# Kernel optimization log

Hardware: AMD Instinct MI355X
Metric: run time of the kernel (lower is better)

The kernel has to match this reference:

```python
import math
import jax, jax.numpy as jnp
import numpy as np

EMBED_DIM = 1024
D_K = 1024
D_V = 1024


def setup_inputs() -> dict:
    key = jax.random.key(0)
    ks = jax.random.split(key, 7)
    s = 1.0 / math.sqrt(EMBED_DIM)
    return {
        "x": jax.random.normal(ks[0], (4, 2048, EMBED_DIM), dtype=jnp.float32),
        "Wq": jax.random.normal(ks[1], (EMBED_DIM, D_K), dtype=jnp.float32) * s,
        "bq": jax.random.normal(ks[2], (D_K,), dtype=jnp.float32) * 0.01,
        "Wk": jax.random.normal(ks[3], (EMBED_DIM, D_K), dtype=jnp.float32) * s,
        "bk": jax.random.normal(ks[4], (D_K,), dtype=jnp.float32) * 0.01,
        "Wv": jax.random.normal(ks[5], (EMBED_DIM, D_V), dtype=jnp.float32) * s,
        "bv": jax.random.normal(ks[6], (D_V,), dtype=jnp.float32) * 0.01,
    }


def reference(x, Wq, bq, Wk, bk, Wv, bv):
    # x: [B, S, E]
    q = x @ Wq + bq  # [B, S, Dk]
    k = x @ Wk + bk  # [B, S, Dk]
    v = x @ Wv + bv  # [B, S, Dv]
    scores = jnp.einsum('bqd,bkd->bqk', q, k) / jnp.sqrt(jnp.float32(q.shape[-1]))
    # NOTE: softmax over axis=1 (the QUERY axis), matching torch dim=1 on [B,S,S]
    attn = jax.nn.softmax(scores, axis=1)
    return jnp.einsum('bqk,bkv->bqv', attn, v)  # [B, S, Dv]
```

## Files before the change

### kernel.cpp

```cpp
#include <hip/hip_runtime.h>
#include <math.h>

typedef unsigned short ushort_t;
typedef __attribute__((ext_vector_type(8))) short short8;
typedef __attribute__((ext_vector_type(8))) _Float16 half8;
typedef __attribute__((ext_vector_type(4))) float floatx4;

#define BATCH 4
#define SEQ   2048
#define EMB   1024

#define GBM 128
#define GBN 128
#define GBK 32

__device__ __forceinline__ ushort_t f2bf(float f) {
    unsigned u = __float_as_uint(f);
    u += 0x7fff + ((u >> 16) & 1);
    return (ushort_t)(u >> 16);
}
__device__ __forceinline__ float bf2f(ushort_t h) {
    return __uint_as_float(((unsigned)h) << 16);
}
__device__ __forceinline__ ushort_t f2h_bits(float f) {
    _Float16 h = (_Float16)f;
    return __builtin_bit_cast(ushort_t, h);
}
__device__ __forceinline__ float h2f(ushort_t b) {
    return (float)__builtin_bit_cast(_Float16, b);
}

__device__ __forceinline__ void gl_lds16(const ushort_t* g, ushort_t* l) {
    __builtin_amdgcn_global_load_lds(
        (const __attribute__((address_space(1))) void*)g,
        (__attribute__((address_space(3))) void*)l,
        16, 0, 0);
}

__device__ __forceinline__ float wave_reduce_sum(float v) {
    #pragma unroll
    for (int off = 32; off; off >>= 1) v += __shfl_down(v, off, 64);
    return v;
}

__device__ __forceinline__ void split4(const float* __restrict__ in,
                                       ushort_t* __restrict__ hi,
                                       ushort_t* __restrict__ lo, size_t i)
{
    float4 v = reinterpret_cast<const float4*>(in)[i];
    float vv[4] = {v.x, v.y, v.z, v.w};
    unsigned h[4], l[4];
    #pragma unroll
    for (int j = 0; j < 4; ++j) {
        h[j] = f2bf(vv[j]);
        l[j] = f2bf(vv[j] - bf2f((ushort_t)h[j]));
    }
    uint2 hv, lv;
    hv.x = h[0] | (h[1] << 16); hv.y = h[2] | (h[3] << 16);
    lv.x = l[0] | (l[1] << 16); lv.y = l[2] | (l[3] << 16);
    *reinterpret_cast<uint2*>(hi + i * 4) = hv;
    *reinterpret_cast<uint2*>(lo + i * 4) = lv;
}

__device__ __forceinline__ void gemv_body(const float* __restrict__ A,
                                          const float* __restrict__ xv,
                                          float* __restrict__ out,
                                          int row, int ncols, float scale)
{
    const int lane = threadIdx.x & 63;
    const float4* ap = reinterpret_cast<const float4*>(A + (size_t)row * ncols);
    const float4* xp = reinterpret_cast<const float4*>(xv);
    float s = 0.f;
    for (int j = lane; j < (ncols >> 2); j += 64) {
        float4 av = ap[j], bv = xp[j];
        s += av.x * bv.x + av.y * bv.y + av.z * bv.z + av.w * bv.w;
    }
    s = wave_reduce_sum(s);
    if (lane == 0) out[row] = s * scale;
}

__global__ __launch_bounds__(256)
void preprocess(const float* __restrict__ x, ushort_t* __restrict__ x16,
                const float* __restrict__ Wq, ushort_t* __restrict__ Wqsh, ushort_t* __restrict__ Wqsl,
                const float* __restrict__ Wk, ushort_t* __restrict__ Wksh, ushort_t* __restrict__ Wksl,
                const float* __restrict__ Wv, ushort_t* __restrict__ Wvt16,
                const float* __restrict__ bk, float* __restrict__ uv)
{
    const int bid = blockIdx.x;
    const int tid = threadIdx.x;
    if (bid < 8192) {
        size_t i = (size_t)bid * 256 + tid;
        float4 v = reinterpret_cast<const float4*>(x)[i];
        unsigned q0 = f2h_bits(v.x), q1 = f2h_bits(v.y);
        unsigned q2 = f2h_bits(v.z), q3 = f2h_bits(v.w);
        uint2 qv; qv.x = q0 | (q1 << 16); qv.y = q2 | (q3 << 16);
        *reinterpret_cast<uint2*>(x16 + i * 4) = qv;
    } else if (bid < 9216) {
        split4(Wq, Wqsh, Wqsl, (size_t)(bid - 8192) * 256 + tid);
    } else if (bid < 10240) {
        split4(Wk, Wksh, Wksl, (size_t)(bid - 9216) * 256 + tid);
    } else if (bid < 11264) {
        __shared__ float tile[32][33];
        const int r = bid - 10240;
        const int r0 = (r >> 5) * 32, c0 = (r & 31) * 32;
        const int tr = tid >> 5;
        const int tc = tid & 31;
        #pragma unroll
        for (int rr = 0; rr < 32; rr += 8)
            tile[tr + rr][tc] = Wv[(size_t)(r0 + tr + rr) * EMB + c0 + tc];
        __syncthreads();
        #pragma unroll
        for (int rr = 0; rr < 32; rr += 8) {
            float v = tile[tc][tr + rr] * 32.f;
            size_t o = (size_t)(c0 + tr + rr) * EMB + r0 + tc;
            Wvt16[o] = f2h_bits(v);
        }
    } else {
        const int row = (bid - 11264) * 4 + (tid >> 6);
        gemv_body(Wq, bk, uv, row, EMB, 1.f);
    }
}

template<int BIAS_MODE, int MODE>
__device__ __forceinline__ void gemm_body(
    int bx, int by, int bz,
    const ushort_t* __restrict__ Ahi, const ushort_t* __restrict__ Alo,
    int ldA, size_t bsA,
    const ushort_t* __restrict__ Bhi, const ushort_t* __restrict__ Blo,
    int ldB, size_t bsB,
    ushort_t* __restrict__ Chi, ushort_t* __restrict__ Clo,
    int ldC, size_t bsC,
    int K, float alpha, const float* __restrict__ bias, size_t bsBias,
    float* __restrict__ ZPart)
{
    const size_t zA = (size_t)bz * bsA;
    const size_t zB = (size_t)bz * bsB;
    const size_t zC = (size_t)bz * bsC;
    const float* bp = bias ? bias + (size_t)bz * bsBias : nullptr;

    __shared__ alignas(16) ushort_t As[2][GBM][GBK];
    __shared__ alignas(16) ushort_t Bs[2][GBN][GBK];

    const int t  = threadIdx.x;
    const int m0 = by * GBM;
    const int n0 = bx * GBN;

    const int sr = t >> 2;
    const int sk = (t & 3) * 8;

    const int lane = t & 63;
    const int wid  = t >> 6;
    const int wm = (wid & 1) * 64;
    const int wn = (wid >> 1) * 64;
    const int fr = lane & 15;
    const int fq = lane >> 4;

    ushort_t* As0 = &As[0][0][0] + wid * 512;
    ushort_t* As1 = &As[1][0][0] + wid * 512;
    ushort_t* Bs0 = &Bs[0][0][0] + wid * 512;
    ushort_t* Bs1 = &Bs[1][0][0] + wid * 512;

    floatx4 acc[4][4];
    #pragma unroll
    for (int i = 0; i < 4; ++i)
        #pragma unroll
        for (int j = 0; j < 4; ++j)
            #pragma unroll
            for (int r = 0; r < 4; ++r) acc[i][j][r] = 0.f;

    for (int k0 = 0; k0 < K; k0 += GBK) {
        const size_t aoff = zA + (size_t)(m0 + sr) * ldA + k0 + sk;
        const size_t boff = zB + (size_t)(n0 + sr) * ldB + k0 + sk;
        const size_t astep = (size_t)64 * ldA;
        const size_t bstep = (size_t)64 * ldB;

        __syncthreads();
        gl_lds16(Ahi + aoff,         As0);
        gl_lds16(Ahi + aoff + astep, As0 + 2048);
        gl_lds16(Alo + aoff,         As1);
        gl_lds16(Alo + aoff + astep, As1 + 2048);
        gl_lds16(Bhi + boff,         Bs0);
        gl_lds16(Bhi + boff + bstep, Bs0 + 2048);
        gl_lds16(Blo + boff,         Bs1);
        gl_lds16(Blo + boff + bstep, Bs1 + 2048);
        __syncthreads();

        short8 ah[4], al[4];
        #pragma unroll
        for (int i = 0; i < 4; ++i) {
            ah[i] = *reinterpret_cast<const short8*>(&As[0][wm + i*16 + fr][fq*8]);
            al[i] = *reinterpret_cast<const short8*>(&As[1][wm + i*16 + fr][fq*8]);
        }
        #pragma unroll
        for (int j = 0; j < 4; ++j) {
            short8 bh = *reinterpret_cast<const short8*>(&Bs[0][wn + j*16 + fr][fq*8]);
            short8 bl = *reinterpret_cast<const short8*>(&Bs[1][wn + j*16 + fr][fq*8]);
            #pragma unroll
            for (int i = 0; i < 4; ++i) {
                acc[i][j] = __builtin_amdgcn_mfma_f32_16x16x32_bf16(ah[i], bh, acc[i][j], 0, 0, 0);
                acc[i][j] = __builtin_amdgcn_mfma_f32_16x16x32_bf16(ah[i], bl, acc[i][j], 0, 0, 0);
                acc[i][j] = __builtin_amdgcn_mfma_f32_16x16x32_bf16(al[i], bh, acc[i][j], 0, 0, 0);
            }
        }
    }

    #pragma unroll
    for (int j = 0; j < 4; ++j) {
        const int col = n0 + wn + j*16 + fr;
        #pragma unroll
        for (int i = 0; i < 4; ++i) {
            #pragma unroll
            for (int r = 0; r < 4; ++r) {
                const int row = m0 + wm + i*16 + fq*4 + r;
                float v = acc[i][j][r] * alpha;
                if (BIAS_MODE == 2) v += bp[row];
                const size_t o = zC + (size_t)row * ldC + col;
                if (MODE == 4) {
                    Chi[o] = f2h_bits(v);
                } else {
                    ushort_t h = f2bf(v);
                    Chi[o] = h;
                    Clo[o] = f2bf(v - bf2f(h));
                }
            }
        }
    }
}

__global__ __launch_bounds__(256)
void mix2(const ushort_t* __restrict__ Wksh, const ushort_t* __restrict__ Wksl,
          const ushort_t* __restrict__ Wqsh, const ushort_t* __restrict__ Wqsl,
          ushort_t* __restrict__ Mt16,
          const float* __restrict__ x, const float* __restrict__ uv,
          float* __restrict__ av)
{
    const int bid = blockIdx.x;
    if (bid < 64) {
        gemm_body<0, 4>(bid & 7, bid >> 3, 0,
            Wksh, Wksl, EMB, 0, Wqsh, Wqsl, EMB, 0,
            Mt16, nullptr, EMB, 0, EMB, 32.f, nullptr, 0, nullptr);
    } else {
        const int row = (bid - 64) * 4 + (threadIdx.x >> 6);
        gemv_body(x, uv, av, row, EMB, 0.03125f);
    }
}

template<int MODE>
__device__ __forceinline__ void f16ss_body(
    int bx, int by, int bz, int gridY,
    const ushort_t* __restrict__ Ah, int ldA, size_t bsA,
    const ushort_t* __restrict__ Bh, int ldB, size_t bsB,
    float* __restrict__ C, ushort_t* __restrict__ Ch,
    int ldC, size_t bsC,
    int K, float alpha, const float* __restrict__ bias, size_t bsBias,
    float* __restrict__ ZPart)
{
    const size_t zA = (size_t)bz * bsA;
    const size_t zB = (size_t)bz * bsB;
    const size_t zC = (size_t)bz * bsC;
    const float* bp = bias ? bias + (size_t)bz * bsBias : nullptr;

    __shared__ alignas(16) ushort_t As[2][GBM][32];
    __shared__ alignas(16) ushort_t Bs[2][GBN][32];

    const int t  = threadIdx.x;
    const int m0 = by * GBM;
    const int n0 = bx * GBN;

    const int sr = t >> 2;
    const int sk = (t & 3) * 8;

    const int lane = t & 63;
    const int wid  = t >> 6;
    const int wm = (wid & 1) * 64;
    const int wn = (wid >> 1) * 64;
    const int fr = lane & 15;
    const int fq = lane >> 4;

    ushort_t* A0 = &As[0][0][0] + wid * 512;
    ushort_t* A1 = &As[1][0][0] + wid * 512;
    ushort_t* B0 = &Bs[0][0][0] + wid * 512;
    ushort_t* B1 = &Bs[1][0][0] + wid * 512;

    floatx4 acc[4][4];
    #pragma unroll
    for (int i = 0; i < 4; ++i)
        #pragma unroll
        for (int j = 0; j < 4; ++j)
            #pragma unroll
            for (int r = 0; r < 4; ++r) acc[i][j][r] = 0.f;

    for (int k0 = 0; k0 < K; k0 += 64) {
        const size_t aoff = zA + (size_t)(m0 + sr) * ldA + k0 + sk;
        const size_t boff = zB + (size_t)(n0 + sr) * ldB + k0 + sk;
        const size_t astep = (size_t)64 * ldA;
        const size_t bstep = (size_t)64 * ldB;

        __syncthreads();
        gl_lds16(Ah + aoff,              A0);
        gl_lds16(Ah + aoff + astep,      A0 + 2048);
        gl_lds16(Ah + aoff + 32,         A1);
        gl_lds16(Ah + aoff + 32 + astep, A1 + 2048);
        gl_lds16(Bh + boff,              B0);
        gl_lds16(Bh + boff + bstep,      B0 + 2048);
        gl_lds16(Bh + boff + 32,         B1);
        gl_lds16(Bh + boff + 32 + bstep, B1 + 2048);
        __syncthreads();

        half8 a[2][4];
        #pragma unroll
        for (int p = 0; p < 2; ++p)
            #pragma unroll
            for (int i = 0; i < 4; ++i)
                a[p][i] = *reinterpret_cast<const half8*>(&As[p][wm + i*16 + fr][fq*8]);
        #pragma unroll
        for (int j = 0; j < 4; ++j) {
            #pragma unroll
            for (int p = 0; p < 2; ++p) {
                half8 bh = *reinterpret_cast<const half8*>(&Bs[p][wn + j*16 + fr][fq*8]);
                #pragma unroll
                for (int i = 0; i < 4; ++i)
                    acc[i][j] = __builtin_amdgcn_mfma_f32_16x16x32_f16(a[p][i], bh, acc[i][j], 0, 0, 0);
            }
        }
    }

    if (MODE == 1) {
        __shared__ float sZ[4][4][16];
        #pragma unroll
        for (int j = 0; j < 4; ++j) {
            const int col = n0 + wn + j*16 + fr;
            float Zloc = 0.f;
            #pragma unroll
            for (int i = 0; i < 4; ++i) {
                #pragma unroll
                for (int r = 0; r < 4; ++r) {
                    const int row = m0 + wm + i*16 + fq*4 + r;
                    float v = acc[i][j][r] * alpha + bp[row];
                    float p = __expf(v);
                    ushort_t hb = f2h_bits(p);
                    Ch[zC + (size_t)row * ldC + col] = hb;
                    Zloc += h2f(hb);
                }
            }
            Zloc += __shfl_xor(Zloc, 16, 64);
            Zloc += __shfl_xor(Zloc, 32, 64);
            if (fq == 0) sZ[wid][j][fr] = Zloc;
        }
        __syncthreads();
        if ((wid & 1) == 0 && fq == 0) {
            #pragma unroll
            for (int j = 0; j < 4; ++j) {
                float Zc = sZ[wid][j][fr] + sZ[wid + 1][j][fr];
                const int col = n0 + wn + j*16 + fr;
                size_t o = ((size_t)bz * gridY + by) * ldC + col;
                ZPart[o] = Zc;
            }
        }
    } else {
        #pragma unroll
        for (int j = 0; j < 4; ++j) {
            const int col = n0 + wn + j*16 + fr;
            #pragma unroll
            for (int i = 0; i < 4; ++i) {
                #pragma unroll
                for (int r = 0; r < 4; ++r) {
                    const int row = m0 + wm + i*16 + fq*4 + r;
                    float v = acc[i][j][r] * alpha;
                    const size_t o = zC + (size_t)row * ldC + col;
                    if (MODE == 0) {
                        C[o] = v;
                    } else if (MODE == 2) {
                        Ch[o] = f2h_bits(v);
                    } else {
                        Ch[o] = f2h_bits(v + bp[row]);
                    }
                }
            }
        }
    }
}

__global__ __launch_bounds__(256)
void tv_gemm(const ushort_t* __restrict__ x16, const ushort_t* __restrict__ Mt16,
             ushort_t* __restrict__ t16,
             const ushort_t* __restrict__ Wvt16, ushort_t* __restrict__ Vraw,
             const float* __restrict__ bv)
{
    const int bid = blockIdx.x;
    if (bid < 512) {
        int f = bid;
        int swz = (f & 7) * 64 + (f >> 3);
        f16ss_body<2>(swz & 7, swz >> 3, 0, 1, x16, EMB, 0, Mt16, EMB, 0,
            nullptr, t16, EMB, 0, EMB, 1.f / 32.f, nullptr, 0, nullptr);
    } else {
        int f = bid - 512;
        int swz = (f & 7) * 64 + (f >> 3);
        f16ss_body<5>(swz & 63, swz >> 6, 0, 1, Wvt16, EMB, 0, x16, EMB, 0,
            nullptr, Vraw, BATCH * SEQ, 0, EMB, 1.f / 32.f, bv, 0, nullptr);
    }
}

__global__ __launch_bounds__(256)
void scores_k(const ushort_t* __restrict__ t16, const ushort_t* __restrict__ x16,
              ushort_t* __restrict__ Pm, const float* __restrict__ av,
              float* __restrict__ ZPart)
{
    const int S = SEQ;
    int f = blockIdx.x + 16 * (blockIdx.y + 16 * blockIdx.z);
    int swz = (f & 7) * 128 + (f >> 3);
    int bx = swz & 15, by = (swz >> 4) & 15, bz = swz >> 8;
    f16ss_body<1>(bx, by, bz, 16, t16, EMB, (size_t)S * EMB,
        x16, EMB, (size_t)S * EMB,
        nullptr, Pm, S, (size_t)S * S, EMB, 0.03125f, av, (size_t)S, ZPart);
}

__global__ __launch_bounds__(256)
void vscale(const ushort_t* __restrict__ Vraw, const float* __restrict__ ZP,
            ushort_t* __restrict__ V16)
{
    const int g = blockIdx.x * 256 + threadIdx.x;
    const int b = g >> 11, s = g & (SEQ - 1);
    float Z = 0.f;
    #pragma unroll
    for (int ch = 0; ch < 16; ++ch)
        Z += ZP[(((size_t)b * 16 + ch) << 11) + s];
    const float zv = 8192.0f / Z;
    const int d0 = blockIdx.y * 64;
    for (int r = 0; r < 64; ++r) {
        size_t o = (size_t)(d0 + r) * (BATCH * SEQ) + g;
        V16[o] = f2h_bits(h2f(Vraw[o]) * zv);
    }
}

__global__ __launch_bounds__(256)
void pv_k(const ushort_t* __restrict__ Pm, const ushort_t* __restrict__ V16,
          float* __restrict__ out)
{
    const int S = SEQ;
    int f = blockIdx.x + 8 * (blockIdx.y + 16 * blockIdx.z);
    int swz = (f & 7) * 64 + (f >> 3);
    int bx = swz & 7, by = (swz >> 3) & 15, bz = swz >> 7;
    f16ss_body<0>(bx, by, bz, 16, Pm, S, (size_t)S * S,
        V16, BATCH * SEQ, (size_t)S,
        out, nullptr, EMB, (size_t)S * EMB, S, 1.f / 8192.f, nullptr, 0, nullptr);
}

extern "C" void kernel_launch(void* const* d_in, const int* in_sizes, int n_in,
                              void* d_out, int out_size, void* d_ws, size_t ws_size,
                              hipStream_t stream)
{
    const float* x  = (const float*)d_in[0];
    const float* Wq = (const float*)d_in[1];
    const float* bq = (const float*)d_in[2];
    const float* Wk = (const float*)d_in[3];
    const float* bk = (const float*)d_in[4];
    const float* Wv = (const float*)d_in[5];
    const float* bv = (const float*)d_in[6];
    (void)bq;

    const int S = SEQ, E = EMB;
    const size_t MT = (size_t)BATCH * S;
    const size_t MB = 1024 * 1024;

    char* base = (char*)d_ws;
    ushort_t* x16   = (ushort_t*)(base +   0 * MB);
    ushort_t* t16   = (ushort_t*)(base +  16 * MB);
    ushort_t* Pm    = (ushort_t*)(base +  32 * MB);
    ushort_t* Vraw  = (ushort_t*)(base +  64 * MB);
    ushort_t* V16   = (ushort_t*)(base +  80 * MB);
    ushort_t* Wvt16 = (ushort_t*)(base +  96 * MB);
    ushort_t* Wqsh  = (ushort_t*)(base +  98 * MB);
    ushort_t* Wqsl  = (ushort_t*)(base + 100 * MB);
    ushort_t* Wksh  = (ushort_t*)(base + 102 * MB);
    ushort_t* Wksl  = (ushort_t*)(base + 104 * MB);
    ushort_t* Mt16  = (ushort_t*)(base + 106 * MB);
    float* uv = (float*)(base + 112 * MB);
    float* av = uv + E;
    float* ZP = av + MT;

    dim3 blk(256);

    preprocess<<<11520, blk, 0, stream>>>(x, x16, Wq, Wqsh, Wqsl,
        Wk, Wksh, Wksl, Wv, Wvt16, bk, uv);

    mix2<<<64 + (unsigned)(MT / 4), blk, 0, stream>>>(
        Wksh, Wksl, Wqsh, Wqsl, Mt16, x, uv, av);

    tv_gemm<<<1024, blk, 0, stream>>>(x16, Mt16, t16, Wvt16, Vraw, bv);

    dim3 gs(S / GBN, S / GBM, BATCH);
    scores_k<<<gs, blk, 0, stream>>>(t16, x16, Pm, av, ZP);

    dim3 gv(32, 16);
    vscale<<<gv, blk, 0, stream>>>(Vraw, ZP, V16);

    dim3 go(E / GBN, S / GBM, BATCH);
    pv_k<<<go, blk, 0, stream>>>(Pm, V16, (float*)d_out);
}
```

Before: 272.9 us.

## Move V projection into mix kernel to overlap with Wk·Wq GEMM and gemv

```diff
diff --git a/kernel.cpp b/kernel.cpp
--- a/kernel.cpp
+++ b/kernel.cpp
@@ -123,23 +123,19 @@
 
 template<int BIAS_MODE, int MODE>
 __device__ __forceinline__ void gemm_body(
-    int bx, int by, int bz,
+    int bx, int by, int bz, ushort_t* smem,
     const ushort_t* __restrict__ Ahi, const ushort_t* __restrict__ Alo,
     int ldA, size_t bsA,
     const ushort_t* __restrict__ Bhi, const ushort_t* __restrict__ Blo,
     int ldB, size_t bsB,
     ushort_t* __restrict__ Chi, ushort_t* __restrict__ Clo,
     int ldC, size_t bsC,
-    int K, float alpha, const float* __restrict__ bias, size_t bsBias,
-    float* __restrict__ ZPart)
+    int K, float alpha, const float* __restrict__ bias, size_t bsBias)
 {
     const size_t zA = (size_t)bz * bsA;
     const size_t zB = (size_t)bz * bsB;
     const size_t zC = (size_t)bz * bsC;
     const float* bp = bias ? bias + (size_t)bz * bsBias : nullptr;
-
-    __shared__ alignas(16) ushort_t As[2][GBM][GBK];
-    __shared__ alignas(16) ushort_t Bs[2][GBN][GBK];
 
     const int t  = threadIdx.x;
     const int m0 = by * GBM;
@@ -155,10 +151,10 @@
     const int fr = lane & 15;
     const int fq = lane >> 4;
 
-    ushort_t* As0 = &As[0][0][0] + wid * 512;
-    ushort_t* As1 = &As[1][0][0] + wid * 512;
-    ushort_t* Bs0 = &Bs[0][0][0] + wid * 512;
-    ushort_t* Bs1 = &Bs[1][0][0] + wid * 512;
+    ushort_t* As0 = smem         + wid * 512;
+    ushort_t* As1 = smem + 4096  + wid * 512;
+    ushort_t* Bs0 = smem + 8192  + wid * 512;
+    ushort_t* Bs1 = smem + 12288 + wid * 512;
 
     floatx4 acc[4][4];
     #pragma unroll
@@ -188,13 +184,13 @@
         short8 ah[4], al[4];
         #pragma unroll
         for (int i = 0; i < 4; ++i) {
-            ah[i] = *reinterpret_cast<const short8*>(&As[0][wm + i*16 + fr][fq*8]);
-            al[i] = *reinterpret_cast<const short8*>(&As[1][wm + i*16 + fr][fq*8]);
+            ah[i] = *reinterpret_cast<const short8*>(smem + (size_t)(wm + i*16 + fr) * GBK + fq*8);
+            al[i] = *reinterpret_cast<const short8*>(smem + 4096 + (size_t)(wm + i*16 + fr) * GBK + fq*8);
         }
         #pragma unroll
         for (int j = 0; j < 4; ++j) {
-            short8 bh = *reinterpret_cast<const short8*>(&Bs[0][wn + j*16 + fr][fq*8]);
-            short8 bl = *reinterpret_cast<const short8*>(&Bs[1][wn + j*16 + fr][fq*8]);
+            short8 bh = *reinterpret_cast<const short8*>(smem + 8192  + (size_t)(wn + j*16 + fr) * GBK + fq*8);
+            short8 bl = *reinterpret_cast<const short8*>(smem + 12288 + (size_t)(wn + j*16 + fr) * GBK + fq*8);
             #pragma unroll
             for (int i = 0; i < 4; ++i) {
                 acc[i][j] = __builtin_amdgcn_mfma_f32_16x16x32_bf16(ah[i], bh, acc[i][j], 0, 0, 0);
@@ -227,27 +223,9 @@
     }
 }
 
-__global__ __launch_bounds__(256)
-void mix2(const ushort_t* __restrict__ Wksh, const ushort_t* __restrict__ Wksl,
-          const ushort_t* __restrict__ Wqsh, const ushort_t* __restrict__ Wqsl,
-          ushort_t* __restrict__ Mt16,
-          const float* __restrict__ x, const float* __restrict__ uv,
-          float* __restrict__ av)
-{
-    const int bid = blockIdx.x;
-    if (bid < 64) {
-        gemm_body<0, 4>(bid & 7, bid >> 3, 0,
-            Wksh, Wksl, EMB, 0, Wqsh, Wqsl, EMB, 0,
-            Mt16, nullptr, EMB, 0, EMB, 32.f, nullptr, 0, nullptr);
-    } else {
-        const int row = (bid - 64) * 4 + (threadIdx.x >> 6);
-        gemv_body(x, uv, av, row, EMB, 0.03125f);
-    }
-}
-
 template<int MODE>
 __device__ __forceinline__ void f16ss_body(
-    int bx, int by, int bz, int gridY,
+    int bx, int by, int bz, int gridY, ushort_t* smem,
     const ushort_t* __restrict__ Ah, int ldA, size_t bsA,
     const ushort_t* __restrict__ Bh, int ldB, size_t bsB,
     float* __restrict__ C, ushort_t* __restrict__ Ch,
@@ -260,8 +238,7 @@
     const size_t zC = (size_t)bz * bsC;
     const float* bp = bias ? bias + (size_t)bz * bsBias : nullptr;
 
-    __shared__ alignas(16) ushort_t As[2][GBM][32];
-    __shared__ alignas(16) ushort_t Bs[2][GBN][32];
+    __shared__ float sZ[MODE == 1 ? 256 : 1];
 
     const int t  = threadIdx.x;
     const int m0 = by * GBM;
@@ -277,10 +254,10 @@
     const int fr = lane & 15;
     const int fq = lane >> 4;
 
-    ushort_t* A0 = &As[0][0][0] + wid * 512;
-    ushort_t* A1 = &As[1][0][0] + wid * 512;
-    ushort_t* B0 = &Bs[0][0][0] + wid * 512;
-    ushort_t* B1 = &Bs[1][0][0] + wid * 512;
+    ushort_t* A0 = smem         + wid * 512;
+    ushort_t* A1 = smem + 4096  + wid * 512;
+    ushort_t* B0 = smem + 8192  + wid * 512;
+    ushort_t* B1 = smem + 12288 + wid * 512;
 
     floatx4 acc[4][4];
     #pragma unroll
@@ -312,12 +289,12 @@
         for (int p = 0; p < 2; ++p)
             #pragma unroll
             for (int i = 0; i < 4; ++i)
-                a[p][i] = *reinterpret_cast<const half8*>(&As[p][wm + i*16 + fr][fq*8]);
+                a[p][i] = *reinterpret_cast<const half8*>(smem + p*4096 + (size_t)(wm + i*16 + fr) * 32 + fq*8);
         #pragma unroll
         for (int j = 0; j < 4; ++j) {
             #pragma unroll
             for (int p = 0; p < 2; ++p) {
-                half8 bh = *reinterpret_cast<const half8*>(&Bs[p][wn + j*16 + fr][fq*8]);
+                half8 bh = *reinterpret_cast<const half8*>(smem + 8192 + p*4096 + (size_t)(wn + j*16 + fr) * 32 + fq*8);
                 #pragma unroll
                 for (int i = 0; i < 4; ++i)
                     acc[i][j] = __builtin_amdgcn_mfma_f32_16x16x32_f16(a[p][i], bh, acc[i][j], 0, 0, 0);
@@ -326,7 +303,6 @@
     }
 
     if (MODE == 1) {
-        __shared__ float sZ[4][4][16];
         #pragma unroll
         for (int j = 0; j < 4; ++j) {
             const int col = n0 + wn + j*16 + fr;
@@ -345,13 +321,13 @@
             }
             Zloc += __shfl_xor(Zloc, 16, 64);
             Zloc += __shfl_xor(Zloc, 32, 64);
-            if (fq == 0) sZ[wid][j][fr] = Zloc;
+            if (fq == 0) sZ[wid * 64 + j * 16 + fr] = Zloc;
         }
         __syncthreads();
         if ((wid & 1) == 0 && fq == 0) {
             #pragma unroll
             for (int j = 0; j < 4; ++j) {
-                float Zc = sZ[wid][j][fr] + sZ[wid + 1][j][fr];
+                float Zc = sZ[wid * 64 + j * 16 + fr] + sZ[(wid + 1) * 64 + j * 16 + fr];
                 const int col = n0 + wn + j*16 + fr;
                 size_t o = ((size_t)bz * gridY + by) * ldC + col;
                 ZPart[o] = Zc;
@@ -382,23 +358,40 @@
 }
 
 __global__ __launch_bounds__(256)
-void tv_gemm(const ushort_t* __restrict__ x16, const ushort_t* __restrict__ Mt16,
-             ushort_t* __restrict__ t16,
-             const ushort_t* __restrict__ Wvt16, ushort_t* __restrict__ Vraw,
-             const float* __restrict__ bv)
-{
+void mix3(const ushort_t* __restrict__ Wksh, const ushort_t* __restrict__ Wksl,
+          const ushort_t* __restrict__ Wqsh, const ushort_t* __restrict__ Wqsl,
+          ushort_t* __restrict__ Mt16,
+          const float* __restrict__ x, const float* __restrict__ uv,
+          float* __restrict__ av,
+          const ushort_t* __restrict__ Wvt16, const ushort_t* __restrict__ x16,
+          ushort_t* __restrict__ Vraw, const float* __restrict__ bv)
+{
+    __shared__ alignas(16) ushort_t smem[16384];
     const int bid = blockIdx.x;
-    if (bid < 512) {
-        int f = bid;
+    if (bid < 64) {
+        gemm_body<0, 4>(bid & 7, bid >> 3, 0, smem,
+            Wksh, Wksl, EMB, 0, Wqsh, Wqsl, EMB, 0,
+            Mt16, nullptr, EMB, 0, EMB, 32.f, nullptr, 0);
+    } else if (bid < 2112) {
+        const int row = (bid - 64) * 4 + (threadIdx.x >> 6);
+        gemv_body(x, uv, av, row, EMB, 0.03125f);
+    } else {
+        int f = bid - 2112;
         int swz = (f & 7) * 64 + (f >> 3);
-        f16ss_body<2>(swz & 7, swz >> 3, 0, 1, x16, EMB, 0, Mt16, EMB, 0,
-            nullptr, t16, EMB, 0, EMB, 1.f / 32.f, nullptr, 0, nullptr);
-    } else {
-        int f = bid - 512;
-        int swz = (f & 7) * 64 + (f >> 3);
-        f16ss_body<5>(swz & 63, swz >> 6, 0, 1, Wvt16, EMB, 0, x16, EMB, 0,
+        f16ss_body<5>(swz & 63, swz >> 6, 0, 1, smem, Wvt16, EMB, 0, x16, EMB, 0,
             nullptr, Vraw, BATCH * SEQ, 0, EMB, 1.f / 32.f, bv, 0, nullptr);
     }
+}
+
+__global__ __launch_bounds__(256)
+void t_k(const ushort_t* __restrict__ x16, const ushort_t* __restrict__ Mt16,
+         ushort_t* __restrict__ t16)
+{
+    __shared__ alignas(16) ushort_t smem[16384];
+    int f = blockIdx.x;
+    int swz = (f & 7) * 64 + (f >> 3);
+    f16ss_body<2>(swz & 7, swz >> 3, 0, 1, smem, x16, EMB, 0, Mt16, EMB, 0,
+        nullptr, t16, EMB, 0, EMB, 1.f / 32.f, nullptr, 0, nullptr);
 }
 
 __global__ __launch_bounds__(256)
@@ -406,11 +399,12 @@
               ushort_t* __restrict__ Pm, const float* __restrict__ av,
               float* __restrict__ ZPart)
 {
+    __shared__ alignas(16) ushort_t smem[16384];
     const int S = SEQ;
     int f = blockIdx.x + 16 * (blockIdx.y + 16 * blockIdx.z);
     int swz = (f & 7) * 128 + (f >> 3);
     int bx = swz & 15, by = (swz >> 4) & 15, bz = swz >> 8;
-    f16ss_body<1>(bx, by, bz, 16, t16, EMB, (size_t)S * EMB,
+    f16ss_body<1>(bx, by, bz, 16, smem, t16, EMB, (size_t)S * EMB,
         x16, EMB, (size_t)S * EMB,
         nullptr, Pm, S, (size_t)S * S, EMB, 0.03125f, av, (size_t)S, ZPart);
 }
@@ -437,11 +431,12 @@
 void pv_k(const ushort_t* __restrict__ Pm, const ushort_t* __restrict__ V16,
           float* __restrict__ out)
 {
+    __shared__ alignas(16) ushort_t smem[16384];
     const int S = SEQ;
     int f = blockIdx.x + 8 * (blockIdx.y + 16 * blockIdx.z);
     int swz = (f & 7) * 64 + (f >> 3);
     int bx = swz & 7, by = (swz >> 3) & 15, bz = swz >> 7;
-    f16ss_body<0>(bx, by, bz, 16, Pm, S, (size_t)S * S,
+    f16ss_body<0>(bx, by, bz, 16, smem, Pm, S, (size_t)S * S,
         V16, BATCH * SEQ, (size_t)S,
         out, nullptr, EMB, (size_t)S * EMB, S, 1.f / 8192.f, nullptr, 0, nullptr);
 }
@@ -484,10 +479,10 @@
     preprocess<<<11520, blk, 0, stream>>>(x, x16, Wq, Wqsh, Wqsl,
         Wk, Wksh, Wksl, Wv, Wvt16, bk, uv);
 
-    mix2<<<64 + (unsigned)(MT / 4), blk, 0, stream>>>(
-        Wksh, Wksl, Wqsh, Wqsl, Mt16, x, uv, av);
-
-    tv_gemm<<<1024, blk, 0, stream>>>(x16, Mt16, t16, Wvt16, Vraw, bv);
+    mix3<<<2624, blk, 0, stream>>>(Wksh, Wksl, Wqsh, Wqsl, Mt16,
+        x, uv, av, Wvt16, x16, Vraw, bv);
+
+    t_k<<<512, blk, 0, stream>>>(x16, Mt16, t16);
 
     dim3 gs(S / GBN, S / GBM, BATCH);
     scores_k<<<gs, blk, 0, stream>>>(t16, x16, Pm, av, ZP);
```

New measurement: 259.9 us. 4.8% less time.
